# Kernel optimization log

Hardware: AMD Instinct MI355X
Metric: run time of the kernel (lower is better)

The kernel has to match this reference:

```python
import jax, jax.numpy as jnp
import numpy as np

N = 50000       # nodes
E = 800000      # edges
IN = 64         # input node feature dim
H = 4           # attention heads
C = 32          # per-head channels (h_dim)
HC = H * C      # 128, concat output per conv
ED = 16         # edge feature dim
G = 2000        # number of graphs (molecules)
NEG = 0.2       # GATConv negative slope


def setup_inputs() -> dict:
    key = jax.random.key(0)
    ks = jax.random.split(key, 40)
    rn = lambda k, shp, s=0.1: (jax.random.normal(k, shp, jnp.float32) * s)
    inp = {}
    inp["x"] = jax.random.normal(ks[0], (N, IN), jnp.float32)
    inp["edge_index"] = jax.random.randint(ks[1], (2, E), 0, N)
    inp["edge_attr"] = jax.random.normal(ks[2], (E, ED), jnp.float32)
    inp["batch"] = jnp.sort(jax.random.randint(ks[3], (N,), 0, G))
    dins = [IN, HC, HC]
    i = 4
    for l in (1, 2, 3):
        din = dins[l - 1]
        inp[f"W{l}"] = rn(ks[i], (din, HC)); i += 1
        inp[f"as{l}"] = rn(ks[i], (H, C)); i += 1
        inp[f"ad{l}"] = rn(ks[i], (H, C)); i += 1
        inp[f"We{l}"] = rn(ks[i], (ED, HC)); i += 1
        inp[f"ae{l}"] = rn(ks[i], (H, C)); i += 1
        inp[f"b{l}"] = rn(ks[i], (HC,)); i += 1
    D = 4 * HC
    inp["lw1"] = rn(ks[i], (D, D)); i += 1
    inp["lb1"] = rn(ks[i], (D,)); i += 1
    inp["lw2"] = rn(ks[i], (D, 1)); i += 1
    inp["lb2"] = rn(ks[i], (1,)); i += 1
    return inp


def gat_conv(x, src, dst, edge_attr, W, a_s, a_d, We, a_e, b):
    n = x.shape[0]
    h = (x @ W).reshape(n, H, C)                       # [N,H,C]
    alpha_src = (h * a_s).sum(-1)                      # [N,H]
    alpha_dst = (h * a_d).sum(-1)                      # [N,H]
    he = (edge_attr @ We).reshape(-1, H, C)            # [E,H,C]
    alpha_edge = (he * a_e).sum(-1)                    # [E,H]
    alpha = jax.nn.leaky_relu(alpha_src[src] + alpha_dst[dst] + alpha_edge, NEG)
    # per-destination softmax over incoming edges (stable)
    amax = jax.ops.segment_max(alpha, dst, num_segments=n)
    amax = jnp.where(jnp.isfinite(amax), amax, 0.0)
    ex = jnp.exp(alpha - amax[dst])                    # [E,H]
    denom = jax.ops.segment_sum(ex, dst, num_segments=n)
    w = ex / (denom[dst] + 1e-16)                      # [E,H]
    m = h[src] * w[:, :, None]                         # [E,H,C]
    out = jax.ops.segment_sum(m, dst, num_segments=n)  # [N,H,C]
    return out.reshape(n, HC) + b


def reference(x, edge_index, edge_attr, batch,
              W1, as1, ad1, We1, ae1, b1,
              W2, as2, ad2, We2, ae2, b2,
              W3, as3, ad3, We3, ae3, b3,
              lw1, lb1, lw2, lb2):
    src, dst = edge_index[0], edge_index[1]
    h1 = gat_conv(x, src, dst, edge_attr, W1, as1, ad1, We1, ae1, b1)
    h2 = gat_conv(h1, src, dst, edge_attr, W2, as2, ad2, We2, ae2, b2)
    h3 = gat_conv(h2, src, dst, edge_attr, W3, as3, ad3, We3, ae3, b3)
    h_pool = jax.ops.segment_sum(h3, batch, num_segments=G)  # global_add_pool
    h_pool_ = h_pool[batch]                                  # == repeat_interleave by counts
    h = jnp.concatenate([h1, h2, h3, h_pool_], axis=1)       # [N, 4*HC]
    h = jax.nn.leaky_relu(h @ lw1 + lb1, 0.01)               # torch LeakyReLU default
    return h @ lw2 + lb2                                     # [N, 1]
```

## Files before the change

kernel.cpp:

```cpp
#include <hip/hip_runtime.h>
#include <hip/hip_bf16.h>
#include <math.h>

#define NN 50000
#define NNP 50048
#define NE 800000
#define DIN1 64
#define NHEAD 4
#define CH 32
#define HC 128
#define EDIM 16
#define NG 2000
#define MAXCH 64

typedef __attribute__((ext_vector_type(8))) short short8;
typedef __attribute__((ext_vector_type(4))) float floatx4;

__device__ __forceinline__ float lrelu(float x, float s) { return x > 0.f ? x : s * x; }

__device__ __forceinline__ unsigned short f2bf(float x) {
  unsigned int u = __float_as_uint(x);
  u += 0x7fff + ((u >> 16) & 1);
  return (unsigned short)(u >> 16);
}
__device__ __forceinline__ float bflo(unsigned int u) { return __uint_as_float(u << 16); }
__device__ __forceinline__ float bfhi(unsigned int u) { return __uint_as_float(u & 0xffff0000u); }

__device__ __forceinline__ void async16(void* lds, const void* g) {
  __builtin_amdgcn_global_load_lds((const __attribute__((address_space(1))) unsigned int*)g,
                                   (__attribute__((address_space(3))) unsigned int*)lds, 16, 0, 0);
}

#define NB_WEA 1
#define NB_WSD 24
#define NB_LW1T 768
#define NB_WT 160
#define NB_CAST 12500
#define NB_GST 196
#define NB_OUT 196
#define NB_HIST 3125
#define PREP_BLOCKS (NB_WEA + NB_WSD + NB_LW1T + NB_WT + NB_CAST + NB_GST + NB_OUT + NB_HIST)

__global__ __launch_bounds__(256) void k_prep(
    const float* __restrict__ We1, const float* __restrict__ ae1,
    const float* __restrict__ We2, const float* __restrict__ ae2,
    const float* __restrict__ We3, const float* __restrict__ ae3, float* __restrict__ wea,
    const float* __restrict__ W1, const float* __restrict__ as1, const float* __restrict__ ad1,
    const float* __restrict__ W2, const float* __restrict__ as2, const float* __restrict__ ad2,
    const float* __restrict__ W3, const float* __restrict__ as3, const float* __restrict__ ad3,
    unsigned short* __restrict__ wsdb,
    const float* __restrict__ lw1, unsigned short* __restrict__ lw1img,
    unsigned short* __restrict__ wtb,
    const float* __restrict__ x, unsigned short* __restrict__ xb0,
    const int* __restrict__ batch, int* __restrict__ gs,
    float* __restrict__ out, const float* __restrict__ lb2,
    const int* __restrict__ dstp, int* __restrict__ cnt) {
  int b = blockIdx.x;
  int t = threadIdx.x;
  if (b < NB_WEA) {
    if (t >= 3 * EDIM * NHEAD) return;
    int l = t / (EDIM * NHEAD);
    int rem = t % (EDIM * NHEAD);
    int d = rem / NHEAD, h = rem % NHEAD;
    const float* We = (l == 0) ? We1 : ((l == 1) ? We2 : We3);
    const float* ae = (l == 0) ? ae1 : ((l == 1) ? ae2 : ae3);
    float s = 0.f;
    for (int c = 0; c < CH; ++c) s += We[d * HC + h * CH + c] * ae[h * CH + c];
    wea[t] = s;
    return;
  }
  b -= NB_WEA;
  if (b < NB_WSD) {
    int i = b * 256 + t;
    int l = i >> 11;
    int col = (i >> 7) & 15;
    int k = i & 127;
    size_t oidx = (size_t)l * 2048 + ((size_t)(k >> 3) * 16 + col) * 8 + (k & 7);
    if (col >= 8 || (l == 0 && k >= DIN1)) { wsdb[oidx] = 0; return; }
    const float* W = (l == 0) ? W1 : ((l == 1) ? W2 : W3);
    int head = col & 3;
    const float* av = (col < 4) ? ((l == 0) ? as1 : ((l == 1) ? as2 : as3))
                                : ((l == 0) ? ad1 : ((l == 1) ? ad2 : ad3));
    float s = 0.f;
    for (int c = 0; c < CH; ++c) s += W[(size_t)k * HC + head * CH + c] * av[head * CH + c];
    wsdb[oidx] = f2bf(s);
    return;
  }
  b -= NB_WSD;
  if (b < NB_LW1T) {
    int i = b * 256 + t;
    int j = i / 384, k = i % 384;
    int jh = j >> 8, jc = j & 255;
    lw1img[((size_t)jh * 48 * 256 + (size_t)(k >> 3) * 256 + jc) * 8 + (k & 7)] =
        f2bf(lw1[(size_t)k * 512 + j]);
    return;
  }
  b -= NB_LW1T;
  if (b < NB_WT) {
    int i = b * 256 + t;
    const float* W;
    int j, k;
    size_t base;
    if (i < 128 * 64) {
      W = W1; j = i / 64; k = i % 64; base = 0;
    } else if (i < 128 * 64 + 128 * 128) {
      int ii = i - 128 * 64;
      W = W2; j = ii / 128; k = ii % 128; base = 8192;
    } else {
      int ii = i - (128 * 64 + 128 * 128);
      W = W3; j = ii / 128; k = ii % 128; base = 24576;
    }
    wtb[base + ((size_t)(k >> 3) * 128 + j) * 8 + (k & 7)] = f2bf(W[(size_t)k * HC + j]);
    return;
  }
  b -= NB_WT;
  if (b < NB_CAST) {
    int i = b * 256 + t;
    int n = i >> 6, k = i & 63;
    xb0[((size_t)(k >> 3) * NNP + n) * 8 + (k & 7)] = f2bf(x[i]);
    return;
  }
  b -= NB_CAST;
  if (b < NB_GST) {
    int i = b * 256 + t;
    if (i >= NN) return;
    int bb = batch[i];
    if (i == 0) {
      for (int g = 0; g <= bb; ++g) gs[g] = 0;
    } else {
      int pb = batch[i - 1];
      for (int g = pb + 1; g <= bb; ++g) gs[g] = i;
    }
    if (i == NN - 1) {
      for (int g = bb + 1; g <= NG; ++g) gs[g] = NN;
    }
    return;
  }
  b -= NB_GST;
  if (b < NB_OUT) {
    int i = b * 256 + t;
    if (i < NN) out[i] = lb2[0];
    return;
  }
  b -= NB_OUT;
  {
    int e = b * 256 + t;
    if (e < NE) atomicAdd(&cnt[dstp[e]], 1);
  }
}

__global__ __launch_bounds__(256) void k_scan1(const int* __restrict__ cnt, int* __restrict__ row_start,
                                               int* __restrict__ aux) {
  __shared__ int s[256];
  int t = threadIdx.x;
  int i = blockIdx.x * 256 + t;
  int v = (i < NN) ? cnt[i] : 0;
  s[t] = v;
  __syncthreads();
  for (int off = 1; off < 256; off <<= 1) {
    int tv = (t >= off) ? s[t - off] : 0;
    __syncthreads();
    s[t] += tv;
    __syncthreads();
  }
  if (i < NN) row_start[i] = s[t] - v;
  if (t == 255) aux[blockIdx.x] = s[255];
}

__global__ __launch_bounds__(256) void k_scan2(int* __restrict__ aux, int nb) {
  __shared__ int s[256];
  int t = threadIdx.x;
  int v = (t < nb) ? aux[t] : 0;
  s[t] = v;
  __syncthreads();
  for (int off = 1; off < 256; off <<= 1) {
    int tv = (t >= off) ? s[t - off] : 0;
    __syncthreads();
    s[t] += tv;
    __syncthreads();
  }
  if (t < nb) aux[t] = s[t] - v;
}

__global__ __launch_bounds__(256) void k_scan3(int* __restrict__ row_start, const int* __restrict__ aux) {
  int i = blockIdx.x * 256 + threadIdx.x;
  if (i < NN) row_start[i] += aux[i >> 8];
  else if (i == NN) row_start[NN] = NE;
}

__global__ __launch_bounds__(256) void k_scatter(const int* __restrict__ dst, const int* __restrict__ row_start,
                                                 int* __restrict__ fill, int* __restrict__ perm) {
  int e = blockIdx.x * 256 + threadIdx.x;
  if (e >= NE) return;
  int d = dst[e];
  int p = atomicAdd(&fill[d], 1);
  perm[row_start[d] + p] = e;
}

__global__ __launch_bounds__(256) void k_permute(const int* __restrict__ perm, const int* __restrict__ src,
                                                 const float* __restrict__ edge_attr, const float* __restrict__ wea,
                                                 int* __restrict__ srcp, float* __restrict__ aep) {
  __shared__ float wl[3 * EDIM * NHEAD];
  int t = threadIdx.x;
  if (t < 3 * EDIM * NHEAD) wl[t] = wea[t];
  __syncthreads();
  int pos = blockIdx.x * 256 + t;
  if (pos >= NE) return;
  int e = perm[pos];
  srcp[pos] = src[e];
  float ea[EDIM];
#pragma unroll
  for (int k = 0; k < EDIM; k += 4) {
    float4 v = *(const float4*)&edge_attr[(size_t)e * EDIM + k];
    ea[k] = v.x; ea[k + 1] = v.y; ea[k + 2] = v.z; ea[k + 3] = v.w;
  }
#pragma unroll
  for (int l = 0; l < 3; ++l) {
    float a0 = 0.f, a1 = 0.f, a2 = 0.f, a3 = 0.f;
#pragma unroll
    for (int k = 0; k < EDIM; ++k) {
      float ev = ea[k];
      a0 += ev * wl[l * 64 + k * 4 + 0];
      a1 += ev * wl[l * 64 + k * 4 + 1];
      a2 += ev * wl[l * 64 + k * 4 + 2];
      a3 += ev * wl[l * 64 + k * 4 + 3];
    }
    *(float4*)&aep[(size_t)l * NE * 4 + (size_t)pos * 4] = make_float4(a0, a1, a2, a3);
  }
}

template <int K>
__global__ __launch_bounds__(256) void k_conv_mfma(const unsigned short* __restrict__ xin,
                                                   const unsigned short* __restrict__ wt,
                                                   const unsigned short* __restrict__ wsd,
                                                   unsigned short* __restrict__ htb,
                                                   float* __restrict__ asrc, float* __restrict__ adst) {
  constexpr int NC = K / 8;
  constexpr int CA = NC * 128;
  constexpr int CB2 = NC * 16;
  __shared__ unsigned short As[CA * 8];
  __shared__ unsigned short Bs[CA * 8];
  __shared__ unsigned short Bs2[CB2 * 8];
  int t = threadIdx.x;
  int n0 = blockIdx.x * 128;
  int lane = t & 63;
  int wave = t >> 6;
  int wr = wave >> 1, wc = wave & 1;

  floatx4 acc[4][4];
  floatx4 acce[4];
#pragma unroll
  for (int a = 0; a < 4; ++a) {
    acce[a] = (floatx4){0.f, 0.f, 0.f, 0.f};
#pragma unroll
    for (int b = 0; b < 4; ++b) acc[a][b] = (floatx4){0.f, 0.f, 0.f, 0.f};
  }

  for (int c0 = wave * 64; c0 < CA; c0 += 256) {
    int kc = c0 >> 7, row0 = c0 & 127;
    async16(As + (size_t)c0 * 8, xin + ((size_t)kc * NNP + n0 + row0 + lane) * 8);
    async16(Bs + (size_t)c0 * 8, wt + ((size_t)c0 + lane) * 8);
  }
  if (wave * 64 < CB2) async16(Bs2 + (size_t)wave * 64 * 8, wsd + ((size_t)wave * 64 + lane) * 8);

  __syncthreads();

  int frow = lane & 15, fkc = lane >> 4;
#pragma unroll
  for (int kk = 0; kk < K / 32; ++kk) {
    const unsigned short* ab = As + (size_t)(kk * 4 + fkc) * 128 * 8;
    const unsigned short* bb = Bs + (size_t)(kk * 4 + fkc) * 128 * 8;
    short8 af[4], bf[4], bf2;
#pragma unroll
    for (int ti = 0; ti < 4; ++ti) af[ti] = *(const short8*)(ab + ((size_t)(wr * 64 + frow + ti * 16)) * 8);
#pragma unroll
    for (int tj = 0; tj < 4; ++tj) bf[tj] = *(const short8*)(bb + ((size_t)(wc * 64 + frow + tj * 16)) * 8);
    bf2 = *(const short8*)(Bs2 + ((size_t)(kk * 4 + fkc) * 16 + frow) * 8);
#pragma unroll
    for (int ti = 0; ti < 4; ++ti)
#pragma unroll
      for (int tj = 0; tj < 4; ++tj)
        acc[ti][tj] = __builtin_amdgcn_mfma_f32_16x16x32_bf16(af[ti], bf[tj], acc[ti][tj], 0, 0, 0);
    if (wc == 0) {
#pragma unroll
      for (int ti = 0; ti < 4; ++ti)
        acce[ti] = __builtin_amdgcn_mfma_f32_16x16x32_bf16(af[ti], bf2, acce[ti], 0, 0, 0);
    }
  }

  int q = lane & 15;
  int colg = wc * 64 + q;
#pragma unroll
  for (int ti = 0; ti < 4; ++ti) {
    int rowb = n0 + wr * 64 + ti * 16 + (lane >> 4) * 4;
#pragma unroll
    for (int r = 0; r < 4; ++r) {
      int row = rowb + r;
      if (row < NN) {
        htb[(size_t)row * HC + colg] = f2bf(acc[ti][0][r]);
        htb[(size_t)row * HC + colg + 16] = f2bf(acc[ti][1][r]);
        htb[(size_t)row * HC + colg + 32] = f2bf(acc[ti][2][r]);
        htb[(size_t)row * HC + colg + 48] = f2bf(acc[ti][3][r]);
        if (wc == 0 && q < 8) {
          float v = acce[ti][r];
          if (q < 4) asrc[row * 4 + q] = v;
          else adst[row * 4 + (q - 4)] = v;
        }
      }
    }
  }
}

__global__ __launch_bounds__(256) void k_aggregate(
    const unsigned short* __restrict__ htb, const int* __restrict__ srcp,
    const float* __restrict__ aep, const float* __restrict__ asrc, const float* __restrict__ adst,
    const int* __restrict__ row_start, const float* __restrict__ bias,
    unsigned short* __restrict__ XBp, int kcoff) {
  __shared__ float exs[4][MAXCH][4];
  int t = threadIdx.x;
  int lane = t & 63, wid = t >> 6;
  int n = blockIdx.x * 4 + wid;
  if (n >= NN) return;
  int rs = row_start[n], re = row_start[n + 1];
  int nchunk = (re - rs + MAXCH - 1) / MAXCH;
  int q = lane & 15, g = lane >> 4;
  int h = q >> 2;
  float4 ad4 = *(const float4*)&adst[n * 4];
  float acc[8];
#pragma unroll
  for (int j = 0; j < 8; ++j) acc[j] = 0.f;
  float d0 = 0.f, d1 = 0.f, d2 = 0.f, d3 = 0.f;

  for (int cc = 0; cc < nchunk; ++cc) {
    int base = rs + cc * MAXCH;
    int m = re - base;
    if (m > MAXCH) m = MAXCH;
    if (lane < m) {
      int i = base + lane;
      int s = srcp[i];
      float4 ae = *(const float4*)&aep[(size_t)i * 4];
      float4 as4 = *(const float4*)&asrc[s * 4];
      float4 ex;
      ex.x = __expf(lrelu(as4.x + ad4.x + ae.x, 0.2f));
      ex.y = __expf(lrelu(as4.y + ad4.y + ae.y, 0.2f));
      ex.z = __expf(lrelu(as4.z + ad4.z + ae.z, 0.2f));
      ex.w = __expf(lrelu(as4.w + ad4.w + ae.w, 0.2f));
      *(float4*)&exs[wid][lane][0] = ex;
      d0 += ex.x; d1 += ex.y; d2 += ex.z; d3 += ex.w;
    }
    __threadfence_block();
    int iters = (m + 7) >> 3;
    for (int kk = 0; kk < iters; ++kk) {
      int ii0 = kk * 8 + g;
      int ii1 = ii0 + 4;
      int i0 = base + ((ii0 < m) ? ii0 : 0);
      int i1 = base + ((ii1 < m) ? ii1 : 0);
      int s0 = srcp[i0];
      int s1 = srcp[i1];
      uint4 h0 = *(const uint4*)(htb + (size_t)s0 * HC + q * 8);
      uint4 h1 = *(const uint4*)(htb + (size_t)s1 * HC + q * 8);
      float w0 = (ii0 < m) ? exs[wid][ii0][h] : 0.f;
      float w1 = (ii1 < m) ? exs[wid][ii1][h] : 0.f;
      acc[0] += w0 * bflo(h0.x) + w1 * bflo(h1.x);
      acc[1] += w0 * bfhi(h0.x) + w1 * bfhi(h1.x);
      acc[2] += w0 * bflo(h0.y) + w1 * bflo(h1.y);
      acc[3] += w0 * bfhi(h0.y) + w1 * bfhi(h1.y);
      acc[4] += w0 * bflo(h0.z) + w1 * bflo(h1.z);
      acc[5] += w0 * bfhi(h0.z) + w1 * bfhi(h1.z);
      acc[6] += w0 * bflo(h0.w) + w1 * bflo(h1.w);
      acc[7] += w0 * bfhi(h0.w) + w1 * bfhi(h1.w);
    }
    __threadfence_block();
  }

#pragma unroll
  for (int mm = 1; mm < 64; mm <<= 1) {
    d0 += __shfl_xor(d0, mm, 64);
    d1 += __shfl_xor(d1, mm, 64);
    d2 += __shfl_xor(d2, mm, 64);
    d3 += __shfl_xor(d3, mm, 64);
  }
#pragma unroll
  for (int j = 0; j < 8; ++j) {
    acc[j] += __shfl_xor(acc[j], 16, 64);
    acc[j] += __shfl_xor(acc[j], 32, 64);
  }
  if (g == 0) {
    float dh = (h == 0) ? d0 : ((h == 1) ? d1 : ((h == 2) ? d2 : d3));
    float inv = 1.f / (dh + 1e-16f);
    unsigned int w[4];
#pragma unroll
    for (int j = 0; j < 4; ++j) {
      float v0 = acc[2 * j] * inv + bias[q * 8 + 2 * j];
      float v1 = acc[2 * j + 1] * inv + bias[q * 8 + 2 * j + 1];
      w[j] = (unsigned int)f2bf(v0) | ((unsigned int)f2bf(v1) << 16);
    }
    *(uint4*)&XBp[((size_t)(kcoff + q) * NNP + n) * 8] = make_uint4(w[0], w[1], w[2], w[3]);
  }
}

__global__ __launch_bounds__(128) void k_pool(const unsigned short* __restrict__ XBp, const int* __restrict__ gs,
                                              float* __restrict__ hpool) {
  int g = blockIdx.x;
  int j = threadIdx.x;
  int kc = 32 + (j >> 3), sb = j & 7;
  int s = gs[g], e = gs[g + 1];
  float acc = 0.f;
  for (int i = s; i < e; ++i) acc += bflo((unsigned int)XBp[((size_t)kc * NNP + i) * 8 + sb]);
  hpool[(size_t)g * HC + j] = acc;
}

__global__ __launch_bounds__(256) void k_pool_gemm(const float* __restrict__ hpool, const float* __restrict__ lw1,
                                                   float* __restrict__ ph) {
  __shared__ float hp[16][128];
  int t = threadIdx.x;
  int j0 = blockIdx.x * 128;
  int g0 = blockIdx.y * 16;
  int jj = t & 127, gg = t >> 7;
#pragma unroll
  for (int i = 0; i < 8; ++i) {
    int q = t + 256 * i;
    int row = q >> 7, col = q & 127;
    hp[row][col] = hpool[(size_t)(g0 + row) * HC + col];
  }
  __syncthreads();
  float acc[8];
#pragma unroll
  for (int i = 0; i < 8; ++i) acc[i] = 0.f;
  for (int k = 0; k < HC; ++k) {
    float wv = lw1[(size_t)(384 + k) * 512 + j0 + jj];
#pragma unroll
    for (int gi = 0; gi < 8; ++gi) acc[gi] += hp[gg + 2 * gi][k] * wv;
  }
#pragma unroll
  for (int gi = 0; gi < 8; ++gi) ph[(size_t)(g0 + gg + 2 * gi) * 512 + j0 + jj] = acc[gi];
}

__global__ __launch_bounds__(256, 2) void k_mlp_mfma(
    const unsigned short* __restrict__ XBp, const unsigned short* __restrict__ lw1img,
    const float* __restrict__ ph, const int* __restrict__ batch,
    const float* __restrict__ lb1, const float* __restrict__ lw2,
    float* __restrict__ out) {
  __shared__ unsigned short As[2 * 512 * 8];
  __shared__ unsigned short Bs[2 * 1024 * 8];
  int t = threadIdx.x;
  int jh = blockIdx.x;
  int n0 = blockIdx.y * 128;
  int lane = t & 63;
  int wave = t >> 6;
  int wr = wave >> 1, wc = wave & 1;
  int kadd = wave >> 1, rb = (wave & 1) * 64;
  const unsigned short* bimg = lw1img + (size_t)jh * 48 * 256 * 8;

  floatx4 acc[4][8];
#pragma unroll
  for (int a = 0; a < 4; ++a)
#pragma unroll
    for (int b = 0; b < 8; ++b) acc[a][b] = (floatx4){0.f, 0.f, 0.f, 0.f};

#define STAGE(bufv, kbv)                                                                  \
  do {                                                                                    \
    const int _bf = (bufv);                                                               \
    const int _kb = (kbv);                                                                \
    _Pragma("unroll") for (int pp = 0; pp < 2; ++pp)                                      \
        async16(As + ((size_t)_bf * 512 + pp * 256 + wave * 64) * 8,                      \
                XBp + ((size_t)(_kb + pp * 2 + kadd) * NNP + n0 + rb + lane) * 8);        \
    _Pragma("unroll") for (int pp = 0; pp < 4; ++pp)                                      \
        async16(Bs + ((size_t)_bf * 1024 + pp * 256 + wave * 64) * 8,                     \
                bimg + ((size_t)(_kb + pp) * 256 + wave * 64 + lane) * 8);                \
  } while (0)

  STAGE(0, 0);

  int frow = lane & 15, fkc = lane >> 4;
  for (int kk = 0; kk < 12; ++kk) {
    int p = kk & 1;
    __syncthreads();
    const unsigned short* ab = As + (size_t)p * 512 * 8 + ((size_t)fkc * 128 + wr * 64 + frow) * 8;
    const unsigned short* bb = Bs + (size_t)p * 1024 * 8 + ((size_t)fkc * 256 + wc * 128 + frow) * 8;
    short8 af[4], bf[8];
#pragma unroll
    for (int ti = 0; ti < 4; ++ti) af[ti] = *(const short8*)(ab + (size_t)ti * 16 * 8);
#pragma unroll
    for (int tj = 0; tj < 8; ++tj) bf[tj] = *(const short8*)(bb + (size_t)tj * 16 * 8);
    if (kk < 11) STAGE(1 - p, (kk + 1) * 4);
#pragma unroll
    for (int ti = 0; ti < 4; ++ti)
#pragma unroll
      for (int tj = 0; tj < 8; ++tj)
        acc[ti][tj] = __builtin_amdgcn_mfma_f32_16x16x32_bf16(af[ti], bf[tj], acc[ti][tj], 0, 0, 0);
  }
#undef STAGE

  int colg = jh * 256 + wc * 128 + (lane & 15);
#pragma unroll
  for (int ti = 0; ti < 4; ++ti) {
    int rowb = n0 + wr * 64 + ti * 16 + (lane >> 4) * 4;
#pragma unroll
    for (int r = 0; r < 4; ++r) {
      int row = rowb + r;
      int rc = (row < NN) ? row : 0;
      int bg = batch[rc];
      float partial = 0.f;
#pragma unroll
      for (int tj = 0; tj < 8; ++tj) {
        int j = colg + tj * 16;
        float v = acc[ti][tj][r] + ph[(size_t)bg * 512 + j] + lb1[j];
        partial += lrelu(v, 0.01f) * lw2[j];
      }
#pragma unroll
      for (int m = 1; m < 16; m <<= 1) partial += __shfl_xor(partial, m, 16);
      if ((lane & 15) == 0 && row < NN) atomicAdd(&out[row], partial);
    }
  }
}

extern "C" void kernel_launch(void* const* d_in, const int* in_sizes, int n_in,
                              void* d_out, int out_size, void* d_ws, size_t ws_size,
                              hipStream_t stream) {
  const float* x = (const float*)d_in[0];
  const int* edge_index = (const int*)d_in[1];
  const int* src = edge_index;
  const int* dstp = edge_index + NE;
  const float* edge_attr = (const float*)d_in[2];
  const int* batch = (const int*)d_in[3];
  const float* W[3] = {(const float*)d_in[4], (const float*)d_in[10], (const float*)d_in[16]};
  const float* as_[3] = {(const float*)d_in[5], (const float*)d_in[11], (const float*)d_in[17]};
  const float* ad_[3] = {(const float*)d_in[6], (const float*)d_in[12], (const float*)d_in[18]};
  const float* We_[3] = {(const float*)d_in[7], (const float*)d_in[13], (const float*)d_in[19]};
  const float* ae_[3] = {(const float*)d_in[8], (const float*)d_in[14], (const float*)d_in[20]};
  const float* b_[3] = {(const float*)d_in[9], (const float*)d_in[15], (const float*)d_in[21]};
  const float* lw1 = (const float*)d_in[22];
  const float* lb1 = (const float*)d_in[23];
  const float* lw2 = (const float*)d_in[24];
  const float* lb2 = (const float*)d_in[25];
  float* out = (float*)d_out;

  float* f = (float*)d_ws;
  size_t o = 0;
  float* asrc = f + o;  o += (size_t)NN * NHEAD;
  float* adst = f + o;  o += (size_t)NN * NHEAD;
  float* wea = f + o;   o += 256;
  float* hpool = f + o; o += (size_t)NG * HC;
  float* aep = f + o;   o += (size_t)3 * NE * 4;
  unsigned short* xb0 = (unsigned short*)(f + o);
  float* ph = (float*)xb0;
  o += (size_t)8 * NNP * 8 / 2;
  unsigned short* htb = (unsigned short*)(f + o);   o += (size_t)NN * HC / 2;
  unsigned short* XB = (unsigned short*)(f + o);    o += (size_t)48 * NNP * 8 / 2;
  unsigned short* wtb = (unsigned short*)(f + o);   o += (size_t)(128 * 64 + 2 * 128 * 128) / 2;
  unsigned short* lw1img = (unsigned short*)(f + o); o += (size_t)2 * 48 * 256 * 8 / 2;
  unsigned short* wsdb = (unsigned short*)(f + o);  o += (size_t)3 * 2048 / 2;
  int* row_start = (int*)(f + o);
  int* cnt = row_start + (NN + 1);
  int* fill = cnt + NN;
  int* aux = fill + NN;
  int* gs = aux + 256;
  int* perm = gs + (NG + 1);
  int* srcp = perm + NE;

  const int NB = (NN + 255) / 256;
  const int EB = (NE + 255) / 256;

  hipMemsetAsync(cnt, 0, (size_t)2 * NN * sizeof(int), stream);

  k_prep<<<PREP_BLOCKS, 256, 0, stream>>>(
      We_[0], ae_[0], We_[1], ae_[1], We_[2], ae_[2], wea,
      W[0], as_[0], ad_[0], W[1], as_[1], ad_[1], W[2], as_[2], ad_[2], wsdb,
      lw1, lw1img, wtb, x, xb0, batch, gs, out, lb2, dstp, cnt);
  k_scan1<<<NB, 256, 0, stream>>>(cnt, row_start, aux);
  k_scan2<<<1, 256, 0, stream>>>(aux, NB);
  k_scan3<<<NB, 256, 0, stream>>>(row_start, aux);
  k_scatter<<<EB, 256, 0, stream>>>(dstp, row_start, fill, perm);
  k_permute<<<EB, 256, 0, stream>>>(perm, src, edge_attr, wea, srcp, aep);

  const int CONVB = NNP / 128;
  unsigned short* wt_l[3] = {wtb, wtb + 8192, wtb + 24576};
  for (int l = 0; l < 3; ++l) {
    unsigned short* wsd_l = wsdb + (size_t)l * 2048;
    const unsigned short* xin = (l == 0) ? xb0 : (XB + (size_t)(l - 1) * 16 * NNP * 8);
    if (l == 0)
      k_conv_mfma<64><<<CONVB, 256, 0, stream>>>(xin, wt_l[0], wsd_l, htb, asrc, adst);
    else
      k_conv_mfma<128><<<CONVB, 256, 0, stream>>>(xin, wt_l[l], wsd_l, htb, asrc, adst);
    k_aggregate<<<(NN + 3) / 4, 256, 0, stream>>>(htb, srcp, aep + (size_t)l * NE * 4, asrc, adst,
                                                  row_start, b_[l], XB, l * 16);
  }

  k_pool<<<NG, 128, 0, stream>>>(XB, gs, hpool);
  k_pool_gemm<<<dim3(4, NG / 16), 256, 0, stream>>>(hpool, lw1, ph);
  k_mlp_mfma<<<dim3(2, NNP / 128), 256, 0, stream>>>(XB, lw1img, ph, batch, lb1, lw2, out);
}
```

Baseline: 485.7 us.

## Load MLP MFMA fragments directly from global into registers, dropping LDS staging

The MLP GEMM kernel no longer stages A and B tiles through double-buffered shared memory with async copies and barriers. Each wave now loads its bf16 fragments straight from global memory into registers, using an explicit even/odd register double-buffer so the next k-step's loads can overlap the current MFMAs. This removes LDS traffic and __syncthreads, but waves sharing tiles now fetch them redundantly from global/L2, and register pressure rises under the 2-blocks launch bound.

```diff
diff --git a/kernel.cpp b/kernel.cpp
--- a/kernel.cpp
+++ b/kernel.cpp
@@ -441,15 +441,12 @@
     const float* __restrict__ ph, const int* __restrict__ batch,
     const float* __restrict__ lb1, const float* __restrict__ lw2,
     float* __restrict__ out) {
-  __shared__ unsigned short As[2 * 512 * 8];
-  __shared__ unsigned short Bs[2 * 1024 * 8];
   int t = threadIdx.x;
   int jh = blockIdx.x;
   int n0 = blockIdx.y * 128;
   int lane = t & 63;
   int wave = t >> 6;
   int wr = wave >> 1, wc = wave & 1;
-  int kadd = wave >> 1, rb = (wave & 1) * 64;
   const unsigned short* bimg = lw1img + (size_t)jh * 48 * 256 * 8;
 
   floatx4 acc[4][8];
@@ -458,39 +455,40 @@
 #pragma unroll
     for (int b = 0; b < 8; ++b) acc[a][b] = (floatx4){0.f, 0.f, 0.f, 0.f};
 
-#define STAGE(bufv, kbv)                                                                  \
-  do {                                                                                    \
-    const int _bf = (bufv);                                                               \
-    const int _kb = (kbv);                                                                \
-    _Pragma("unroll") for (int pp = 0; pp < 2; ++pp)                                      \
-        async16(As + ((size_t)_bf * 512 + pp * 256 + wave * 64) * 8,                      \
-                XBp + ((size_t)(_kb + pp * 2 + kadd) * NNP + n0 + rb + lane) * 8);        \
-    _Pragma("unroll") for (int pp = 0; pp < 4; ++pp)                                      \
-        async16(Bs + ((size_t)_bf * 1024 + pp * 256 + wave * 64) * 8,                     \
-                bimg + ((size_t)(_kb + pp) * 256 + wave * 64 + lane) * 8);                \
-  } while (0)
-
-  STAGE(0, 0);
-
-  int frow = lane & 15, fkc = lane >> 4;
-  for (int kk = 0; kk < 12; ++kk) {
-    int p = kk & 1;
-    __syncthreads();
-    const unsigned short* ab = As + (size_t)p * 512 * 8 + ((size_t)fkc * 128 + wr * 64 + frow) * 8;
-    const unsigned short* bb = Bs + (size_t)p * 1024 * 8 + ((size_t)fkc * 256 + wc * 128 + frow) * 8;
-    short8 af[4], bf[8];
-#pragma unroll
-    for (int ti = 0; ti < 4; ++ti) af[ti] = *(const short8*)(ab + (size_t)ti * 16 * 8);
-#pragma unroll
-    for (int tj = 0; tj < 8; ++tj) bf[tj] = *(const short8*)(bb + (size_t)tj * 16 * 8);
-    if (kk < 11) STAGE(1 - p, (kk + 1) * 4);
+  const unsigned short* abase = XBp + (((size_t)(lane >> 4)) * NNP + n0 + wr * 64 + (lane & 15)) * 8;
+  const unsigned short* bbase = bimg + (((size_t)(lane >> 4)) * 256 + wc * 128 + (lane & 15)) * 8;
+  const size_t akk = (size_t)4 * NNP * 8;
+  const size_t bkk = (size_t)4 * 256 * 8;
+
+  short8 af0[4], af1[4], bfE[8], bfO[8];
+#pragma unroll
+  for (int ti = 0; ti < 4; ++ti) af0[ti] = *(const short8*)(abase + (size_t)ti * 16 * 8);
+
+#pragma unroll
+  for (int kk2 = 0; kk2 < 6; ++kk2) {
+    const unsigned short* ae_ = abase + (size_t)(2 * kk2) * akk;
+    const unsigned short* be_ = bbase + (size_t)(2 * kk2) * bkk;
+#pragma unroll
+    for (int tj = 0; tj < 8; ++tj) bfE[tj] = *(const short8*)(be_ + (size_t)tj * 16 * 8);
+#pragma unroll
+    for (int ti = 0; ti < 4; ++ti) af1[ti] = *(const short8*)(ae_ + akk + (size_t)ti * 16 * 8);
 #pragma unroll
     for (int ti = 0; ti < 4; ++ti)
 #pragma unroll
       for (int tj = 0; tj < 8; ++tj)
-        acc[ti][tj] = __builtin_amdgcn_mfma_f32_16x16x32_bf16(af[ti], bf[tj], acc[ti][tj], 0, 0, 0);
-  }
-#undef STAGE
+        acc[ti][tj] = __builtin_amdgcn_mfma_f32_16x16x32_bf16(af0[ti], bfE[tj], acc[ti][tj], 0, 0, 0);
+#pragma unroll
+    for (int tj = 0; tj < 8; ++tj) bfO[tj] = *(const short8*)(be_ + bkk + (size_t)tj * 16 * 8);
+    if (kk2 < 5) {
+#pragma unroll
+      for (int ti = 0; ti < 4; ++ti) af0[ti] = *(const short8*)(ae_ + 2 * akk + (size_t)ti * 16 * 8);
+    }
+#pragma unroll
+    for (int ti = 0; ti < 4; ++ti)
+#pragma unroll
+      for (int tj = 0; tj < 8; ++tj)
+        acc[ti][tj] = __builtin_amdgcn_mfma_f32_16x16x32_bf16(af1[ti], bfO[tj], acc[ti][tj], 0, 0, 0);
+  }
 
   int colg = jh * 256 + wc * 128 + (lane & 15);
 #pragma unroll
```

Measured after the change: 491.0 us. No clear change (+1.1%).
